# Performance work log

Hardware: AMD Instinct MI355X
Metric: run time of the kernel (lower is better)

The kernel has to match this reference:

```python
import math
import jax, jax.numpy as jnp
import numpy as np

NUM_HEADS = 16
NUM_LANDMARKS = 64
INV_ITERS = 6
ATT_SIZE = 1024
HEAD_SIZE = ATT_SIZE // NUM_HEADS  # dk = 64
NEG = -100000.0


def moore_penrose_pinv(x, num_iter):
    # lucidrains-style iterative Moore-Penrose pseudo-inverse
    abs_x = jnp.abs(x)
    col = abs_x.sum(axis=-1)
    row = abs_x.sum(axis=-2)
    z = jnp.swapaxes(x, -1, -2) / (jnp.max(col) * jnp.max(row))
    I = jnp.eye(x.shape[-1], dtype=x.dtype)
    for _ in range(num_iter):
        xz = x @ z
        z = 0.25 * z @ (13.0 * I - xz @ (15.0 * I - xz @ (7.0 * I - xz)))
    return z


def masked_softmax_scores(k, q, mask):
    # q @ k^T (dk=1: q already scaled) + mask, softmax over last dim
    s = jnp.einsum('bhmd,bhld->bhml', q, k)
    if mask is not None:
        s = s + (1.0 - mask) * NEG
    return jax.nn.softmax(s, axis=-1)


def setup_inputs() -> dict:
    key = jax.random.key(0)
    k1, k2, k3 = jax.random.split(key, 3)
    B, L, D = 4, 4096, 1024
    x = jax.random.normal(k1, (B, L, D), dtype=jnp.float32)
    attention_mask = jnp.ones((B, L), dtype=jnp.float32)
    w_kqv = jax.random.normal(k2, (3 * ATT_SIZE, D), dtype=jnp.float32) * 0.02
    w_out = jax.random.normal(k3, (ATT_SIZE, ATT_SIZE), dtype=jnp.float32) * 0.02
    b_out = jnp.zeros((ATT_SIZE,), dtype=jnp.float32)
    return {"x": x, "attention_mask": attention_mask,
            "w_kqv": w_kqv, "w_out": w_out, "b_out": b_out}


def reference(x, attention_mask, w_kqv, w_out, b_out):
    B, L, D = x.shape
    H, nl, hd = NUM_HEADS, NUM_LANDMARKS, HEAD_SIZE
    seg = L // nl  # landmark segment length (L already a multiple of nl)

    kqv = x @ w_kqv.T  # [B, L, 3A]
    k, q, v = jnp.split(kqv, 3, axis=-1)
    split = lambda t: t.reshape(B, L, H, hd).transpose(0, 2, 1, 3)  # [B,H,L,hd]
    k, q, v = split(k), split(q), split(v)

    mask = attention_mask[:, None, :]  # [B,1,L]
    denom = mask.reshape(B, 1, nl, seg).sum(-1) + 1e-08  # [B,1,nl]
    mask_lm = (denom > 0).astype(x.dtype)  # [B,1,nl]
    denom4 = denom[..., None]              # [B,1,nl,1]
    maskL = mask[..., None]                # [B,1,L,1]

    q = q * maskL
    k = k * maskL
    v = v * maskL

    s1_mask = maskL * mask_lm[..., None, :]               # [B,1,L,nl]
    s2_mask = mask_lm[..., None] * mask_lm[..., None, :]  # [B,1,nl,nl]
    s3_mask = jnp.swapaxes(s1_mask, -1, -2)               # [B,1,nl,L]

    q = q / math.sqrt(HEAD_SIZE)
    q_lm = q.reshape(B, H, nl, seg, hd).sum(-2) / denom4  # [B,H,nl,hd]
    k_lm = k.reshape(B, H, nl, seg, hd).sum(-2) / denom4

    scores_1 = masked_softmax_scores(k_lm, q, s1_mask)     # [B,H,L,nl]
    scores_2 = masked_softmax_scores(k_lm, q_lm, s2_mask)  # [B,H,nl,nl]
    scores_3 = masked_softmax_scores(k, q_lm, s3_mask)     # [B,H,nl,L]

    z_star = moore_penrose_pinv(scores_2, INV_ITERS)       # [B,H,nl,nl]
    out = scores_1 @ (z_star @ (scores_3 @ v))             # [B,H,L,hd]

    out = out.transpose(0, 2, 1, 3).reshape(B, L, H * hd)  # merge heads
    return out @ w_out.T + b_out
```

## Files before the change

kernel.cpp:

```cpp
#include <hip/hip_runtime.h>
#include <hip/hip_bf16.h>


static constexpr int Bn  = 4;
static constexpr int Ln  = 4096;
static constexpr int Dn  = 1024;
static constexpr int Hn  = 16;
static constexpr int HDn = 64;
static constexpr int NLn = 64;
static constexpr int SEGn = 64;
static constexpr int BHn = Bn * Hn;
static constexpr int Mn  = Bn * Ln;
static constexpr int NCH = 8;
#define NEG_BIG (-100000.0f)

static constexpr size_t OFF_KT  = 0;
static constexpr size_t OFF_QT  = 16777216;
static constexpr size_t OFF_VT  = 33554432;
static constexpr size_t OFF_WOH = 33554432;
static constexpr size_t OFF_WH  = 50331648;
static constexpr size_t OFF_QLM = 50331648;
static constexpr size_t OFF_KLM = 50593792;
static constexpr size_t OFF_S2  = 50855936;
static constexpr size_t OFF_Z   = 51118080;
static constexpr size_t OFF_WM  = 51380224;
static constexpr size_t OFF_PM  = 51642368;
static constexpr size_t OFF_PS  = 51675136;
static constexpr size_t OFF_GM  = 51707904;
static constexpr size_t OFF_XS  = 53477376;
static constexpr size_t OFF_PO  = 53477376;

using bf16x8 = __attribute__((ext_vector_type(8))) short;
using f32x16 = __attribute__((ext_vector_type(16))) float;
using s16x4  = __attribute__((ext_vector_type(4))) short;

__device__ __forceinline__ unsigned short f2bf(float f) {
    unsigned int u = __float_as_uint(f);
    return (unsigned short)((u + 0x7fffu + ((u >> 16) & 1u)) >> 16);
}
__device__ __forceinline__ void cvt8r(const float* fs, bf16x8& hv) {
    #pragma unroll
    for (int e = 0; e < 8; ++e) hv[e] = (short)f2bf(fs[e]);
}
typedef __attribute__((address_space(1))) void gvoid;
typedef __attribute__((address_space(3))) void lvoid;
__device__ __forceinline__ void async16(void* l, const void* g) {
    __builtin_amdgcn_global_load_lds((gvoid*)(size_t)g, (lvoid*)l, 16, 0, 0);
}

__global__ __launch_bounds__(256) void k_pack(
    const float* __restrict__ src, unsigned short* __restrict__ dh, int row0)
{
    __shared__ float Ls[128][33];
    const int rt = blockIdx.x, kt = blockIdx.y;
    const int tid = threadIdx.x;
    #pragma unroll
    for (int p = 0; p < 4; ++p) {
        const int row = p * 32 + (tid >> 3);
        const int c4 = (tid & 7) * 4;
        const float4 v = *(const float4*)&src[(size_t)(row0 + rt * 128 + row) * 1024 + kt * 32 + c4];
        Ls[row][c4 + 0] = v.x; Ls[row][c4 + 1] = v.y;
        Ls[row][c4 + 2] = v.z; Ls[row][c4 + 3] = v.w;
    }
    __syncthreads();
    const size_t tb = (size_t)(rt * 32 + kt) * 4096;
    for (int s = tid; s < 512; s += 256) {
        const int g = s >> 7, kk = (s >> 6) & 1, l = s & 63;
        const int row = g * 32 + (l & 31);
        const int k0 = kk * 16 + ((l >> 5) & 1) * 8;
        bf16x8 hv;
        cvt8r(&Ls[row][k0], hv);
        *(bf16x8*)&dh[tb + s * 8] = hv;
    }
}

#define GEMM4W_CORE(A_, B_, NNB)                                               \
    __shared__ __attribute__((aligned(16))) char smem[16384];                  \
    const int tid = threadIdx.x;                                               \
    const int lane = tid & 63, wid = tid >> 6;                                 \
    const int cpx = gridDim.x >> 3;                                            \
    const int wg = (blockIdx.x & 7) * cpx + (blockIdx.x >> 3);                 \
    const int bm = wg / (NNB), bn = wg % (NNB);                                \
    const int wrow = wid >> 1, wcol = wid & 1;                                 \
    const unsigned short* gsrc =                                               \
        (wid < 2 ? (A_) + (size_t)bm * 131072 : (B_) + (size_t)bn * 131072)    \
        + (wid & 1) * 2048 + lane * 8;                                         \
    char* ldst = smem + wid * 4096;                                            \
    f32x16 acc[2][2] = {};                                                     \
    for (int kt = 0; kt < 32; ++kt) {                                          \
        const unsigned short* g = gsrc + (size_t)kt * 4096;                    \
        __syncthreads();                                                       \
        _Pragma("unroll")                                                      \
        for (int i = 0; i < 4; ++i)                                            \
            async16(ldst + i * 1024, g + i * 512);                             \
        __syncthreads();                                                       \
        _Pragma("unroll")                                                      \
        for (int kk = 0; kk < 2; ++kk) {                                       \
            bf16x8 fa[2], fb[2];                                               \
            _Pragma("unroll")                                                  \
            for (int ti = 0; ti < 2; ++ti) {                                   \
                const int o = (((wrow * 2 + ti) * 2 + kk) << 10) + lane * 16;  \
                fa[ti] = *(const bf16x8*)(smem + o);                           \
            }                                                                  \
            _Pragma("unroll")                                                  \
            for (int tj = 0; tj < 2; ++tj) {                                   \
                const int o = (((wcol * 2 + tj) * 2 + kk) << 10) + lane * 16;  \
                fb[tj] = *(const bf16x8*)(smem + 8192 + o);                    \
            }                                                                  \
            _Pragma("unroll")                                                  \
            for (int ti = 0; ti < 2; ++ti)                                     \
                _Pragma("unroll")                                              \
                for (int tj = 0; tj < 2; ++tj)                                 \
                    acc[ti][tj] = __builtin_amdgcn_mfma_f32_32x32x16_bf16(     \
                        fa[ti], fb[tj], acc[ti][tj], 0, 0, 0);                 \
        }                                                                      \
    }

__global__ __launch_bounds__(256) void k_kqv_gemm(
    const unsigned short* __restrict__ xh,
    const unsigned short* __restrict__ wh,
    const float* __restrict__ mask,
    float* __restrict__ Kt, float* __restrict__ Qt, float* __restrict__ Vt,
    int row0)
{
    GEMM4W_CORE(xh, wh, 24)
    const int part = bn >> 3;
    #pragma unroll
    for (int ti = 0; ti < 2; ++ti) {
        #pragma unroll
        for (int tj = 0; tj < 2; ++tj) {
            const int col = (bn * 128 + wcol * 64 + tj * 32 + (lane & 31)) & 1023;
            const int h = col >> 6, d = col & 63;
            #pragma unroll
            for (int r = 0; r < 16; ++r) {
                const int row = row0 + bm * 128 + wrow * 64 + ti * 32
                              + (r & 3) + 8 * (r >> 2) + 4 * (lane >> 5);
                const int b = row >> 12, l = row & 4095;
                const float mk = mask[b * Ln + l];
                const size_t idx = ((size_t)(b * Hn + h) * Ln + l) * HDn + d;
                const float v = acc[ti][tj][r] * mk;
                if (part == 0)      Kt[idx] = v;
                else if (part == 1) Qt[idx] = v * 0.125f;
                else                Vt[idx] = v;
            }
        }
    }
}

__global__ __launch_bounds__(256) void k_out_gemm(
    const unsigned short* __restrict__ ah_,
    const unsigned short* __restrict__ bh_,
    const float* __restrict__ bias, float* __restrict__ out)
{
    GEMM4W_CORE(ah_, bh_, 8)
    #pragma unroll
    for (int ti = 0; ti < 2; ++ti) {
        #pragma unroll
        for (int tj = 0; tj < 2; ++tj) {
            const int col = bn * 128 + wcol * 64 + tj * 32 + (lane & 31);
            const float bb = bias[col];
            #pragma unroll
            for (int r = 0; r < 16; ++r) {
                const int row = bm * 128 + wrow * 64 + ti * 32
                              + (r & 3) + 8 * (r >> 2) + 4 * (lane >> 5);
                out[(size_t)row * Dn + col] = acc[ti][tj][r] + bb;
            }
        }
    }
}

__global__ __launch_bounds__(64) void k_landmarks(
    const float* __restrict__ Kt, const float* __restrict__ Qt,
    const float* __restrict__ mask,
    float* __restrict__ klm, float* __restrict__ qlm, int* __restrict__ gmax)
{
    const int blk = blockIdx.x;
    const int m = blk & 63, bh = blk >> 6, b = bh >> 4;
    const int d = threadIdx.x;
    if (blk == 0 && d < 2) gmax[d] = 0;
    float mv = mask[b * Ln + m * SEGn + d];
    #pragma unroll
    for (int off = 32; off; off >>= 1) mv += __shfl_down(mv, off);
    const float denom = __shfl(mv, 0) + 1e-8f;
    const float* kp = Kt + ((size_t)bh * Ln + m * SEGn) * HDn + d;
    const float* qp = Qt + ((size_t)bh * Ln + m * SEGn) * HDn + d;
    float sk = 0.f, sq = 0.f;
    for (int j = 0; j < SEGn; ++j) {
        sk += kp[(size_t)j * HDn];
        sq += qp[(size_t)j * HDn];
    }
    klm[((size_t)bh * NLn + m) * HDn + d] = sk / denom;
    qlm[((size_t)bh * NLn + m) * HDn + d] = sq / denom;
}

__global__ __launch_bounds__(64) void k_s2(
    const float* __restrict__ qlm, const float* __restrict__ klm,
    float* __restrict__ s2, int* __restrict__ gmax)
{
    const int bh = blockIdx.x;
    __shared__ float ql[64][65];
    __shared__ float kl[64][65];
    __shared__ float sr[64][65];
    const int t = threadIdx.x;
    for (int idx = t; idx < 4096; idx += 64) {
        ql[idx >> 6][idx & 63] = qlm[(size_t)bh * 4096 + idx];
        kl[idx >> 6][idx & 63] = klm[(size_t)bh * 4096 + idx];
    }
    __syncthreads();
    float mx = -1e30f;
    for (int mp = 0; mp < 64; ++mp) {
        float s = 0.f;
        #pragma unroll 8
        for (int d2 = 0; d2 < 64; ++d2) s = fmaf(ql[t][d2], kl[mp][d2], s);
        sr[t][mp] = s;
        mx = fmaxf(mx, s);
    }
    float sum = 0.f;
    for (int mp = 0; mp < 64; ++mp) {
        const float e = expf(sr[t][mp] - mx);
        sr[t][mp] = e;
        sum += e;
    }
    const float inv = 1.f / sum;
    float rs = 0.f;
    for (int mp = 0; mp < 64; ++mp) {
        const float v = sr[t][mp] * inv;
        sr[t][mp] = v;
        s2[(size_t)bh * 4096 + t * 64 + mp] = v;
        rs += fabsf(v);
    }
    __syncthreads();
    float cs = 0.f;
    for (int mm = 0; mm < 64; ++mm) cs += fabsf(sr[mm][t]);
    float rmax = rs, cmax = cs;
    #pragma unroll
    for (int off = 32; off; off >>= 1) {
        rmax = fmaxf(rmax, __shfl_down(rmax, off));
        cmax = fmaxf(cmax, __shfl_down(cmax, off));
    }
    if (t == 0) {
        atomicMax(&gmax[0], __float_as_int(rmax));
        atomicMax(&gmax[1], __float_as_int(cmax));
    }
}

template<int SUB>
__device__ __forceinline__ void mm64v(
    float* C, int ldc, const float* Ag, int lda,
    const float* Bm, int ldb, float dg, float scl)
{
    const int tid = threadIdx.x;
    const int tx = tid & 15, ty = tid >> 4;
    const int i0 = ty << 2, j0 = tx << 2;
    float acc[4][4] = {};
    for (int k0 = 0; k0 < 64; k0 += 4) {
        float4 a4[4], b4[4];
        #pragma unroll
        for (int i = 0; i < 4; ++i)
            a4[i] = *(const float4*)&Ag[(size_t)(i0 + i) * lda + k0];
        #pragma unroll
        for (int kk = 0; kk < 4; ++kk)
            b4[kk] = *(const float4*)&Bm[(size_t)(k0 + kk) * ldb + j0];
        if (SUB) {
            #pragma unroll
            for (int kk = 0; kk < 4; ++kk) {
                float* bp = (float*)&b4[kk];
                #pragma unroll
                for (int j = 0; j < 4; ++j)
                    bp[j] = ((k0 + kk == j0 + j) ? dg : 0.0f) - bp[j];
            }
        }
        #pragma unroll
        for (int i = 0; i < 4; ++i) {
            const float* ap = (const float*)&a4[i];
            #pragma unroll
            for (int kk = 0; kk < 4; ++kk) {
                const float* bp = (const float*)&b4[kk];
                #pragma unroll
                for (int j = 0; j < 4; ++j)
                    acc[i][j] = fmaf(ap[kk], bp[j], acc[i][j]);
            }
        }
    }
    __syncthreads();
    #pragma unroll
    for (int i = 0; i < 4; ++i)
        #pragma unroll
        for (int j = 0; j < 4; ++j) C[(size_t)(i0 + i) * ldc + j0 + j] = scl * acc[i][j];
    __syncthreads();
}

__global__ __launch_bounds__(256) void k_pinv_s3v(
    const float* __restrict__ s2, const int* __restrict__ gmax,
    float* __restrict__ zout,
    const float* __restrict__ qlm, const float* __restrict__ Kt,
    const float* __restrict__ Vt, const float* __restrict__ mask,
    float* __restrict__ Opart, float* __restrict__ mpart, float* __restrict__ spart)
{
    __shared__ __attribute__((aligned(16))) char shm[61184];
    const int tid = threadIdx.x;

    if (blockIdx.y == NCH) {
        float (*Zb)[68] = (float(*)[68])(shm);
        float (*XZ)[68] = (float(*)[68])(shm + 17408);
        float (*Tb)[68] = (float(*)[68])(shm + 34816);
        const int bh = blockIdx.x;
        const float* X = s2 + (size_t)bh * 4096;
        const float scale = 1.0f / (__int_as_float(gmax[0]) * __int_as_float(gmax[1]));
        for (int idx = tid; idx < 4096; idx += 256) {
            const int i = idx >> 6, j = idx & 63;
            Zb[i][j] = X[j * 64 + i] * scale;
        }
        __syncthreads();
        for (int it = 0; it < 6; ++it) {
            mm64v<0>(&XZ[0][0], 68, X, 64, &Zb[0][0], 68, 0.f, 1.f);
            mm64v<1>(&Tb[0][0], 68, &XZ[0][0], 68, &XZ[0][0], 68, 7.f, 1.f);
            mm64v<1>(&Tb[0][0], 68, &XZ[0][0], 68, &Tb[0][0], 68, 15.f, 1.f);
            mm64v<1>(&Zb[0][0], 68, &Zb[0][0], 68, &Tb[0][0], 68, 13.f, 0.25f);
        }
        for (int idx = tid; idx < 4096; idx += 256)
            zout[(size_t)bh * 4096 + idx] = Zb[idx >> 6][idx & 63];
        return;
    }

    float (*Sm)[65] = (float(*)[65])(shm);
    float (*Ks)[65] = (float(*)[65])(shm + 16640);
    float (*Vs)[65] = (float(*)[65])(shm + 33280);
    unsigned short* Qp = (unsigned short*)(shm + 49920);
    float (*red)[4]  = (float(*)[4])(shm + 58112);
    float (*red2)[4] = (float(*)[4])(shm + 59136);
    float* rowmax = (float*)(shm + 60160);
    float* rowsum = (float*)(shm + 60416);
    float* fac    = (float*)(shm + 60672);
    float* mrow   = (float*)(shm + 60928);
    const int bh = blockIdx.x, ch = blockIdx.y;
    const int b = bh >> 4;
    const int lane = tid & 63, wid = tid >> 6;
    const int wr = wid >> 1, wc = wid & 1;

    for (int idx = tid; idx < 4096; idx += 256)
        Sm[idx >> 6][idx & 63] = qlm[(size_t)bh * 4096 + idx];
    if (tid < 64) { rowmax[tid] = -1e30f; rowsum[tid] = 0.f; }
    __syncthreads();
    for (int s = tid; s < 512; s += 256) {
        const int g = s >> 8, kc = (s >> 6) & 3, l = s & 63;
        const int row = g * 32 + (l & 31);
        const int k0 = kc * 16 + ((l >> 5) & 1) * 8;
        bf16x8 hv;
        cvt8r(&Sm[row][k0], hv);
        *(bf16x8*)&Qp[s * 8] = hv;
    }
    f32x16 accO = {};
    const int t0beg = ch * (Ln / NCH), t0end = t0beg + (Ln / NCH);
    for (int t0 = t0beg; t0 < t0end; t0 += 64) {
        __syncthreads();
        for (int idx = tid; idx < 4096; idx += 256) {
            const int r = idx >> 6, c2 = idx & 63;
            Ks[r][c2] = Kt[((size_t)bh * Ln + t0 + r) * HDn + c2];
            Vs[r][c2] = Vt[((size_t)bh * Ln + t0 + r) * HDn + c2];
        }
        if (tid < 64) mrow[tid] = mask[b * Ln + t0 + tid];
        __syncthreads();
        f32x16 acc = {};
        #pragma unroll
        for (int kc = 0; kc < 4; ++kc) {
            const bf16x8 a_h = *(const bf16x8*)&Qp[((wr * 4 + kc) * 64 + lane) * 8];
            const int brow = wc * 32 + (lane & 31);
            const int k0 = kc * 16 + (lane >> 5) * 8;
            bf16x8 b_h;
            cvt8r(&Ks[brow][k0], b_h);
            acc = __builtin_amdgcn_mfma_f32_32x32x16_bf16(a_h, b_h, acc, 0, 0, 0);
        }
        #pragma unroll
        for (int r = 0; r < 16; ++r) {
            const int row = wr * 32 + (r & 3) + 8 * (r >> 2) + 4 * (lane >> 5);
            const int col = wc * 32 + (lane & 31);
            Sm[row][col] = acc[r] + (1.f - mrow[col]) * NEG_BIG;
        }
        __syncthreads();
        {
            const int row = tid >> 2, sg = tid & 3, c0 = sg * 16;
            float mx = -1e30f;
            #pragma unroll
            for (int c = 0; c < 16; ++c) mx = fmaxf(mx, Sm[row][c0 + c]);
            red[row][sg] = mx;
            __syncthreads();
            const float nm = fmaxf(rowmax[row],
                fmaxf(fmaxf(red[row][0], red[row][1]), fmaxf(red[row][2], red[row][3])));
            const float f = __expf(rowmax[row] - nm);
            float ps = 0.f;
            #pragma unroll
            for (int c = 0; c < 16; ++c) {
                const float e = __expf(Sm[row][c0 + c] - nm);
                Sm[row][c0 + c] = e;
                ps += e;
            }
            red2[row][sg] = ps;
            __syncthreads();
            if (sg == 0) {
                rowsum[row] = rowsum[row] * f
                    + red2[row][0] + red2[row][1] + red2[row][2] + red2[row][3];
                rowmax[row] = nm;
                fac[row] = f;
            }
        }
        __syncthreads();
        #pragma unroll
        for (int r = 0; r < 16; ++r) {
            const int row = wr * 32 + (r & 3) + 8 * (r >> 2) + 4 * (lane >> 5);
            accO[r] *= fac[row];
        }
        #pragma unroll
        for (int kc = 0; kc < 4; ++kc) {
            const int arow = wr * 32 + (lane & 31);
            const int ak0 = kc * 16 + (lane >> 5) * 8;
            bf16x8 a_h;
            cvt8r(&Sm[arow][ak0], a_h);
            const int bcol = wc * 32 + (lane & 31);
            const int bk0 = kc * 16 + (lane >> 5) * 8;
            float bw[8];
            #pragma unroll
            for (int e = 0; e < 8; ++e) bw[e] = Vs[bk0 + e][bcol];
            bf16x8 b_h;
            cvt8r(bw, b_h);
            accO = __builtin_amdgcn_mfma_f32_32x32x16_bf16(a_h, b_h, accO, 0, 0, 0);
        }
    }
    __syncthreads();
    #pragma unroll
    for (int r = 0; r < 16; ++r) {
        const int row = wr * 32 + (r & 3) + 8 * (r >> 2) + 4 * (lane >> 5);
        Vs[row][wc * 32 + (lane & 31)] = accO[r];
    }
    __syncthreads();
    const size_t ob = (size_t)(bh * NCH + ch) * 4096;
    for (int idx = tid; idx < 4096; idx += 256)
        Opart[ob + idx] = Vs[idx >> 6][idx & 63];
    if (tid < 64) {
        mpart[(bh * NCH + ch) * 64 + tid] = rowmax[tid];
        spart[(bh * NCH + ch) * 64 + tid] = rowsum[tid];
    }
}

__global__ __launch_bounds__(256) void k_mergez(
    const float* __restrict__ Opart, const float* __restrict__ mpart,
    const float* __restrict__ spart, const float* __restrict__ Zs,
    float* __restrict__ Wm)
{
    __shared__ float Sv[64][68];
    __shared__ float Zb[64][68];
    const int bh = blockIdx.x, tid = threadIdx.x;
    for (int idx = tid; idx < 4096; idx += 256)
        Zb[idx >> 6][idx & 63] = Zs[(size_t)bh * 4096 + idx];
    {
        const int r = tid >> 2, c0 = (tid & 3) * 16;
        float e[NCH];
        float M = -1e30f;
        #pragma unroll
        for (int c = 0; c < NCH; ++c) {
            e[c] = mpart[(bh * NCH + c) * 64 + r];
            M = fmaxf(M, e[c]);
        }
        float S = 0.f;
        #pragma unroll
        for (int c = 0; c < NCH; ++c) {
            e[c] = expf(e[c] - M);
            S += spart[(bh * NCH + c) * 64 + r] * e[c];
        }
        const float invS = 1.f / S;
        for (int col = c0; col < c0 + 16; ++col) {
            float o = 0.f;
            #pragma unroll
            for (int c = 0; c < NCH; ++c)
                o += Opart[(size_t)(bh * NCH + c) * 4096 + r * 64 + col] * e[c];
            Sv[r][col] = o * invS;
        }
    }
    __syncthreads();
    const int tx = tid & 15, ty = tid >> 4;
    const int i0 = ty << 2, j0 = tx << 2;
    float acc[4][4] = {};
    for (int k0 = 0; k0 < 64; k0 += 4) {
        float4 a4[4], b4[4];
        #pragma unroll
        for (int i = 0; i < 4; ++i)
            a4[i] = *(const float4*)&Zb[i0 + i][k0];
        #pragma unroll
        for (int kk = 0; kk < 4; ++kk)
            b4[kk] = *(const float4*)&Sv[k0 + kk][j0];
        #pragma unroll
        for (int i = 0; i < 4; ++i) {
            const float* ap = (const float*)&a4[i];
            #pragma unroll
            for (int kk = 0; kk < 4; ++kk) {
                const float* bp = (const float*)&b4[kk];
                #pragma unroll
                for (int j = 0; j < 4; ++j)
                    acc[i][j] = fmaf(ap[kk], bp[j], acc[i][j]);
            }
        }
    }
    #pragma unroll
    for (int i = 0; i < 4; ++i)
        #pragma unroll
        for (int j = 0; j < 4; ++j)
            Wm[(size_t)bh * 4096 + (i0 + i) * 64 + j0 + j] = acc[i][j];
}

__global__ __launch_bounds__(256) void k_attn_out(
    const float* __restrict__ Qt, const float* __restrict__ klm,
    const float* __restrict__ Wm, unsigned short* __restrict__ ah)
{
    const int lt = blockIdx.x;
    const int bh = blockIdx.y;
    const int b = bh >> 4, h = bh & 15;
    __shared__ float Sm[64][65];
    __shared__ float Ks[64][65];
    __shared__ float Ws[64][65];
    __shared__ unsigned short Qp[4096];
    __shared__ float red[64][4], red2[64][4];
    __shared__ float invr[64];
    const int tid = threadIdx.x;
    const int lane = tid & 63, wid = tid >> 6;
    const int wr = wid >> 1, wc = wid & 1;

    for (int idx = tid; idx < 4096; idx += 256) {
        const int r = idx >> 6, c2 = idx & 63;
        Sm[r][c2] = Qt[((size_t)bh * Ln + lt * 64 + r) * HDn + c2];
        Ks[r][c2] = klm[(size_t)bh * 4096 + idx];
        Ws[r][c2] = Wm[(size_t)bh * 4096 + idx];
    }
    __syncthreads();
    for (int s = tid; s < 512; s += 256) {
        const int g = s >> 8, kc = (s >> 6) & 3, l = s & 63;
        const int row = g * 32 + (l & 31);
        const int k0 = kc * 16 + ((l >> 5) & 1) * 8;
        bf16x8 hv;
        cvt8r(&Sm[row][k0], hv);
        *(bf16x8*)&Qp[s * 8] = hv;
    }
    __syncthreads();
    f32x16 acc = {};
    #pragma unroll
    for (int kc = 0; kc < 4; ++kc) {
        const bf16x8 a_h = *(const bf16x8*)&Qp[((wr * 4 + kc) * 64 + lane) * 8];
        const int brow = wc * 32 + (lane & 31);
        const int k0 = kc * 16 + (lane >> 5) * 8;
        bf16x8 b_h;
        cvt8r(&Ks[brow][k0], b_h);
        acc = __builtin_amdgcn_mfma_f32_32x32x16_bf16(a_h, b_h, acc, 0, 0, 0);
    }
    #pragma unroll
    for (int r = 0; r < 16; ++r) {
        const int row = wr * 32 + (r & 3) + 8 * (r >> 2) + 4 * (lane >> 5);
        Sm[row][wc * 32 + (lane & 31)] = acc[r];
    }
    __syncthreads();
    {
        const int row = tid >> 2, sg = tid & 3, c0 = sg * 16;
        float mx = -1e30f;
        #pragma unroll
        for (int c = 0; c < 16; ++c) mx = fmaxf(mx, Sm[row][c0 + c]);
        red[row][sg] = mx;
        __syncthreads();
        mx = fmaxf(fmaxf(red[row][0], red[row][1]), fmaxf(red[row][2], red[row][3]));
        float ps = 0.f;
        #pragma unroll
        for (int c = 0; c < 16; ++c) {
            const float e = __expf(Sm[row][c0 + c] - mx);
            Sm[row][c0 + c] = e;
            ps += e;
        }
        red2[row][sg] = ps;
        __syncthreads();
        if (sg == 0)
            invr[row] = 1.f / (red2[row][0] + red2[row][1] + red2[row][2] + red2[row][3]);
    }
    __syncthreads();
    f32x16 acc2 = {};
    #pragma unroll
    for (int kc = 0; kc < 4; ++kc) {
        const int arow = wr * 32 + (lane & 31);
        const int ak0 = kc * 16 + (lane >> 5) * 8;
        bf16x8 a_h;
        cvt8r(&Sm[arow][ak0], a_h);
        const int bcol = wc * 32 + (lane & 31);
        const int bk0 = kc * 16 + (lane >> 5) * 8;
        float bw[8];
        #pragma unroll
        for (int e = 0; e < 8; ++e) bw[e] = Ws[bk0 + e][bcol];
        bf16x8 b_h;
        cvt8r(bw, b_h);
        acc2 = __builtin_amdgcn_mfma_f32_32x32x16_bf16(a_h, b_h, acc2, 0, 0, 0);
    }
    __syncthreads();
    #pragma unroll
    for (int r = 0; r < 16; ++r) {
        const int row = wr * 32 + (r & 3) + 8 * (r >> 2) + 4 * (lane >> 5);
        Ks[row][wc * 32 + (lane & 31)] = acc2[r];
    }
    __syncthreads();
    const int tx = tid & 15, ty = tid >> 4;
    const int i0 = ty << 2, j0 = tx << 2;
    const int kd = h * 64 + j0;
    const int kt2 = kd >> 5, kc2 = kd & 31;
    const int kk2 = kc2 >> 4, half = (kc2 & 15) >> 3, e0 = kc2 & 7;
    #pragma unroll
    for (int i = 0; i < 4; ++i) {
        const float inv = invr[i0 + i];
        const int gm = b * Ln + lt * 64 + i0 + i;
        const int mt = gm >> 7, g2 = (gm & 127) >> 5, lrow = gm & 31;
        const size_t u = (size_t)(mt * 32 + kt2) * 4096
                       + (size_t)(((g2 * 2 + kk2) * 64 + half * 32 + lrow) * 8 + e0);
        s16x4 hv;
        #pragma unroll
        for (int j = 0; j < 4; ++j)
            hv[j] = (short)f2bf(Ks[i0 + i][j0 + j] * inv);
        *(s16x4*)&ah[u] = hv;
    }
}

extern "C" void kernel_launch(void* const* d_in, const int* in_sizes, int n_in,
                              void* d_out, int out_size, void* d_ws, size_t ws_size,
                              hipStream_t stream)
{
    (void)in_sizes; (void)n_in; (void)out_size;
    const float* x    = (const float*)d_in[0];
    const float* mask = (const float*)d_in[1];
    const float* wkqv = (const float*)d_in[2];
    const float* wout = (const float*)d_in[3];
    const float* bout = (const float*)d_in[4];
    float* out = (float*)d_out;
    float* ws  = (float*)d_ws;

    float* Kt   = ws + OFF_KT;
    float* Qt   = ws + OFF_QT;
    float* Vt   = ws + OFF_VT;
    float* qlm  = ws + OFF_QLM;
    float* klm  = ws + OFF_KLM;
    float* s2   = ws + OFF_S2;
    float* zst  = ws + OFF_Z;
    float* Wm   = ws + OFF_WM;
    int*   gmax = (int*)(ws + OFF_GM);
    float* mpart = ws + OFF_PM;
    float* spart = ws + OFF_PS;
    float* Opart = ws + OFF_PO;
    unsigned short* wh  = (unsigned short*)(ws + OFF_WH);
    unsigned short* woh = (unsigned short*)(ws + OFF_WOH);
    unsigned short* attn_h = (unsigned short*)(ws + OFF_KT);

    int S = 2048;
    if (ws_size >= (size_t)(OFF_XS + 16384 * 512) * 4) S = 16384;
    else if (ws_size >= (size_t)(OFF_XS + 8192 * 512) * 4) S = 8192;
    else if (ws_size >= (size_t)(OFF_XS + 2097152) * 4) S = 4096;
    unsigned short* xhs = (unsigned short*)(ws + OFF_XS);

    k_pack<<<dim3(24, 32), 256, 0, stream>>>(wkqv, wh, 0);
    for (int s = 0; s < Mn / S; ++s) {
        k_pack<<<dim3(S / 128, 32), 256, 0, stream>>>(x, xhs, s * S);
        k_kqv_gemm<<<(S / 128) * 24, 256, 0, stream>>>(
            xhs, wh, mask, Kt, Qt, Vt, s * S);
    }
    k_landmarks<<<BHn * NLn, 64, 0, stream>>>(Kt, Qt, mask, klm, qlm, gmax);
    k_s2<<<BHn, 64, 0, stream>>>(qlm, klm, s2, gmax);
    k_pinv_s3v<<<dim3(BHn, NCH + 1), 256, 0, stream>>>(
        s2, gmax, zst, qlm, Kt, Vt, mask, Opart, mpart, spart);
    k_pack<<<dim3(8, 32), 256, 0, stream>>>(wout, woh, 0);
    k_mergez<<<BHn, 256, 0, stream>>>(Opart, mpart, spart, zst, Wm);
    k_attn_out<<<dim3(Ln / 64, BHn), 256, 0, stream>>>(Qt, klm, Wm, attn_h);
    k_out_gemm<<<128 * 8, 256, 0, stream>>>(attn_h, woh, bout, out);
}
```

Before: 435.5 us.

## Parallelize s2 softmax over 256 threads and amortize attn_out tile loads

k_s2 now runs 256 threads per head, with four threads sharing each row and partial max, sum and abs-sum values reduced through shared memory. It also switches to the fast __expf. k_attn_out processes four 64-row L tiles per block, so the landmark-key and W tiles are loaded into shared memory once per four tiles instead of once per tile. This cuts redundant global loads and launch count, but leaves four times fewer blocks (1024) and adds an extra shared buffer, which may lower occupancy.

```diff
diff --git a/kernel.cpp b/kernel.cpp
--- a/kernel.cpp
+++ b/kernel.cpp
@@ -193,7 +193,7 @@
     qlm[((size_t)bh * NLn + m) * HDn + d] = sq / denom;
 }
 
-__global__ __launch_bounds__(64) void k_s2(
+__global__ __launch_bounds__(256) void k_s2(
     const float* __restrict__ qlm, const float* __restrict__ klm,
     float* __restrict__ s2, int* __restrict__ gmax)
 {
@@ -201,46 +201,69 @@
     __shared__ float ql[64][65];
     __shared__ float kl[64][65];
     __shared__ float sr[64][65];
-    const int t = threadIdx.x;
-    for (int idx = t; idx < 4096; idx += 64) {
+    __shared__ float red[64][4], red2[64][4];
+    __shared__ float rtmp[64], ctmp[64];
+    const int tid = threadIdx.x;
+    for (int idx = tid; idx < 4096; idx += 256) {
         ql[idx >> 6][idx & 63] = qlm[(size_t)bh * 4096 + idx];
         kl[idx >> 6][idx & 63] = klm[(size_t)bh * 4096 + idx];
     }
     __syncthreads();
+    const int row = tid >> 2, sg = tid & 3, c0 = sg * 16;
+    float sv[16];
     float mx = -1e30f;
-    for (int mp = 0; mp < 64; ++mp) {
+    #pragma unroll 4
+    for (int m = 0; m < 16; ++m) {
         float s = 0.f;
         #pragma unroll 8
-        for (int d2 = 0; d2 < 64; ++d2) s = fmaf(ql[t][d2], kl[mp][d2], s);
-        sr[t][mp] = s;
+        for (int d2 = 0; d2 < 64; ++d2) s = fmaf(ql[row][d2], kl[c0 + m][d2], s);
+        sv[m] = s;
         mx = fmaxf(mx, s);
     }
+    red[row][sg] = mx;
+    __syncthreads();
+    mx = fmaxf(fmaxf(red[row][0], red[row][1]), fmaxf(red[row][2], red[row][3]));
     float sum = 0.f;
-    for (int mp = 0; mp < 64; ++mp) {
-        const float e = expf(sr[t][mp] - mx);
-        sr[t][mp] = e;
+    #pragma unroll
+    for (int m = 0; m < 16; ++m) {
+        const float e = __expf(sv[m] - mx);
+        sv[m] = e;
         sum += e;
     }
-    const float inv = 1.f / sum;
+    red2[row][sg] = sum;
+    __syncthreads();
+    const float inv = 1.f / (red2[row][0] + red2[row][1] + red2[row][2] + red2[row][3]);
     float rs = 0.f;
-    for (int mp = 0; mp < 64; ++mp) {
-        const float v = sr[t][mp] * inv;
-        sr[t][mp] = v;
-        s2[(size_t)bh * 4096 + t * 64 + mp] = v;
+    #pragma unroll
+    for (int m = 0; m < 16; ++m) {
+        const float v = sv[m] * inv;
+        sr[row][c0 + m] = v;
+        s2[(size_t)bh * 4096 + row * 64 + c0 + m] = v;
         rs += fabsf(v);
     }
-    __syncthreads();
+    red[row][sg] = rs;
+    __syncthreads();
+    if (sg == 0)
+        rtmp[row] = red[row][0] + red[row][1] + red[row][2] + red[row][3];
     float cs = 0.f;
-    for (int mm = 0; mm < 64; ++mm) cs += fabsf(sr[mm][t]);
-    float rmax = rs, cmax = cs;
-    #pragma unroll
-    for (int off = 32; off; off >>= 1) {
-        rmax = fmaxf(rmax, __shfl_down(rmax, off));
-        cmax = fmaxf(cmax, __shfl_down(cmax, off));
-    }
-    if (t == 0) {
-        atomicMax(&gmax[0], __float_as_int(rmax));
-        atomicMax(&gmax[1], __float_as_int(cmax));
+    #pragma unroll
+    for (int r = 0; r < 16; ++r) cs += fabsf(sr[c0 + r][row]);
+    red2[row][sg] = cs;
+    __syncthreads();
+    if (sg == 0)
+        ctmp[row] = red2[row][0] + red2[row][1] + red2[row][2] + red2[row][3];
+    __syncthreads();
+    if (tid < 64) {
+        float rmax = rtmp[tid], cmax = ctmp[tid];
+        #pragma unroll
+        for (int off = 32; off; off >>= 1) {
+            rmax = fmaxf(rmax, __shfl_down(rmax, off));
+            cmax = fmaxf(cmax, __shfl_down(cmax, off));
+        }
+        if (tid == 0) {
+            atomicMax(&gmax[0], __float_as_int(rmax));
+            atomicMax(&gmax[1], __float_as_int(cmax));
+        }
     }
 }
 
@@ -511,12 +534,13 @@
     const float* __restrict__ Qt, const float* __restrict__ klm,
     const float* __restrict__ Wm, unsigned short* __restrict__ ah)
 {
-    const int lt = blockIdx.x;
+    const int lt0 = blockIdx.x * 4;
     const int bh = blockIdx.y;
     const int b = bh >> 4, h = bh & 15;
     __shared__ float Sm[64][65];
     __shared__ float Ks[64][65];
     __shared__ float Ws[64][65];
+    __shared__ float Ob[64][65];
     __shared__ unsigned short Qp[4096];
     __shared__ float red[64][4], red2[64][4];
     __shared__ float invr[64];
@@ -526,97 +550,106 @@
 
     for (int idx = tid; idx < 4096; idx += 256) {
         const int r = idx >> 6, c2 = idx & 63;
-        Sm[r][c2] = Qt[((size_t)bh * Ln + lt * 64 + r) * HDn + c2];
         Ks[r][c2] = klm[(size_t)bh * 4096 + idx];
         Ws[r][c2] = Wm[(size_t)bh * 4096 + idx];
     }
     __syncthreads();
-    for (int s = tid; s < 512; s += 256) {
-        const int g = s >> 8, kc = (s >> 6) & 3, l = s & 63;
-        const int row = g * 32 + (l & 31);
-        const int k0 = kc * 16 + ((l >> 5) & 1) * 8;
-        bf16x8 hv;
-        cvt8r(&Sm[row][k0], hv);
-        *(bf16x8*)&Qp[s * 8] = hv;
-    }
-    __syncthreads();
-    f32x16 acc = {};
-    #pragma unroll
-    for (int kc = 0; kc < 4; ++kc) {
-        const bf16x8 a_h = *(const bf16x8*)&Qp[((wr * 4 + kc) * 64 + lane) * 8];
-        const int brow = wc * 32 + (lane & 31);
-        const int k0 = kc * 16 + (lane >> 5) * 8;
-        bf16x8 b_h;
-        cvt8r(&Ks[brow][k0], b_h);
-        acc = __builtin_amdgcn_mfma_f32_32x32x16_bf16(a_h, b_h, acc, 0, 0, 0);
-    }
-    #pragma unroll
-    for (int r = 0; r < 16; ++r) {
-        const int row = wr * 32 + (r & 3) + 8 * (r >> 2) + 4 * (lane >> 5);
-        Sm[row][wc * 32 + (lane & 31)] = acc[r];
-    }
-    __syncthreads();
-    {
-        const int row = tid >> 2, sg = tid & 3, c0 = sg * 16;
-        float mx = -1e30f;
-        #pragma unroll
-        for (int c = 0; c < 16; ++c) mx = fmaxf(mx, Sm[row][c0 + c]);
-        red[row][sg] = mx;
-        __syncthreads();
-        mx = fmaxf(fmaxf(red[row][0], red[row][1]), fmaxf(red[row][2], red[row][3]));
-        float ps = 0.f;
-        #pragma unroll
-        for (int c = 0; c < 16; ++c) {
-            const float e = __expf(Sm[row][c0 + c] - mx);
-            Sm[row][c0 + c] = e;
-            ps += e;
-        }
-        red2[row][sg] = ps;
-        __syncthreads();
-        if (sg == 0)
-            invr[row] = 1.f / (red2[row][0] + red2[row][1] + red2[row][2] + red2[row][3]);
-    }
-    __syncthreads();
-    f32x16 acc2 = {};
-    #pragma unroll
-    for (int kc = 0; kc < 4; ++kc) {
-        const int arow = wr * 32 + (lane & 31);
-        const int ak0 = kc * 16 + (lane >> 5) * 8;
-        bf16x8 a_h;
-        cvt8r(&Sm[arow][ak0], a_h);
-        const int bcol = wc * 32 + (lane & 31);
-        const int bk0 = kc * 16 + (lane >> 5) * 8;
-        float bw[8];
-        #pragma unroll
-        for (int e = 0; e < 8; ++e) bw[e] = Ws[bk0 + e][bcol];
-        bf16x8 b_h;
-        cvt8r(bw, b_h);
-        acc2 = __builtin_amdgcn_mfma_f32_32x32x16_bf16(a_h, b_h, acc2, 0, 0, 0);
-    }
-    __syncthreads();
-    #pragma unroll
-    for (int r = 0; r < 16; ++r) {
-        const int row = wr * 32 + (r & 3) + 8 * (r >> 2) + 4 * (lane >> 5);
-        Ks[row][wc * 32 + (lane & 31)] = acc2[r];
-    }
-    __syncthreads();
-    const int tx = tid & 15, ty = tid >> 4;
-    const int i0 = ty << 2, j0 = tx << 2;
-    const int kd = h * 64 + j0;
-    const int kt2 = kd >> 5, kc2 = kd & 31;
-    const int kk2 = kc2 >> 4, half = (kc2 & 15) >> 3, e0 = kc2 & 7;
-    #pragma unroll
-    for (int i = 0; i < 4; ++i) {
-        const float inv = invr[i0 + i];
-        const int gm = b * Ln + lt * 64 + i0 + i;
-        const int mt = gm >> 7, g2 = (gm & 127) >> 5, lrow = gm & 31;
-        const size_t u = (size_t)(mt * 32 + kt2) * 4096
-                       + (size_t)(((g2 * 2 + kk2) * 64 + half * 32 + lrow) * 8 + e0);
-        s16x4 hv;
-        #pragma unroll
-        for (int j = 0; j < 4; ++j)
-            hv[j] = (short)f2bf(Ks[i0 + i][j0 + j] * inv);
-        *(s16x4*)&ah[u] = hv;
+
+    for (int sub = 0; sub < 4; ++sub) {
+        const int lt = lt0 + sub;
+        for (int idx = tid; idx < 4096; idx += 256)
+            Sm[idx >> 6][idx & 63] = Qt[((size_t)bh * Ln + lt * 64 + (idx >> 6)) * HDn + (idx & 63)];
+        __syncthreads();
+        for (int s = tid; s < 512; s += 256) {
+            const int g = s >> 8, kc = (s >> 6) & 3, l = s & 63;
+            const int row = g * 32 + (l & 31);
+            const int k0 = kc * 16 + ((l >> 5) & 1) * 8;
+            bf16x8 hv;
+            cvt8r(&Sm[row][k0], hv);
+            *(bf16x8*)&Qp[s * 8] = hv;
+        }
+        __syncthreads();
+        f32x16 acc = {};
+        #pragma unroll
+        for (int kc = 0; kc < 4; ++kc) {
+            const bf16x8 a_h = *(const bf16x8*)&Qp[((wr * 4 + kc) * 64 + lane) * 8];
+            const int brow = wc * 32 + (lane & 31);
+            const int k0 = kc * 16 + (lane >> 5) * 8;
+            bf16x8 b_h;
+            cvt8r(&Ks[brow][k0], b_h);
+            acc = __builtin_amdgcn_mfma_f32_32x32x16_bf16(a_h, b_h, acc, 0, 0, 0);
+        }
+        #pragma unroll
+        for (int r = 0; r < 16; ++r) {
+            const int row = wr * 32 + (r & 3) + 8 * (r >> 2) + 4 * (lane >> 5);
+            Sm[row][wc * 32 + (lane & 31)] = acc[r];
+        }
+        __syncthreads();
+        {
+            const int row = tid >> 2, sg = tid & 3, c0 = sg * 16;
+            float mx = -1e30f;
+            #pragma unroll
+            for (int c = 0; c < 16; ++c) mx = fmaxf(mx, Sm[row][c0 + c]);
+            red[row][sg] = mx;
+            __syncthreads();
+            mx = fmaxf(fmaxf(red[row][0], red[row][1]), fmaxf(red[row][2], red[row][3]));
+            float ps = 0.f;
+            #pragma unroll
+            for (int c = 0; c < 16; ++c) {
+                const float e = __expf(Sm[row][c0 + c] - mx);
+                Sm[row][c0 + c] = e;
+                ps += e;
+            }
+            red2[row][sg] = ps;
+            __syncthreads();
+            if (sg == 0)
+                invr[row] = 1.f / (red2[row][0] + red2[row][1] + red2[row][2] + red2[row][3]);
+        }
+        __syncthreads();
+        f32x16 acc2 = {};
+        #pragma unroll
+        for (int kc = 0; kc < 4; ++kc) {
+            const int arow = wr * 32 + (lane & 31);
+            const int ak0 = kc * 16 + (lane >> 5) * 8;
+            bf16x8 a_h;
+            cvt8r(&Sm[arow][ak0], a_h);
+            const int bcol = wc * 32 + (lane & 31);
+            const int bk0 = kc * 16 + (lane >> 5) * 8;
+            float bw[8];
+            #pragma unroll
+            for (int e = 0; e < 8; ++e) bw[e] = Ws[bk0 + e][bcol];
+            bf16x8 b_h;
+            cvt8r(bw, b_h);
+            acc2 = __builtin_amdgcn_mfma_f32_32x32x16_bf16(a_h, b_h, acc2, 0, 0, 0);
+        }
+        __syncthreads();
+        #pragma unroll
+        for (int r = 0; r < 16; ++r) {
+            const int row = wr * 32 + (r & 3) + 8 * (r >> 2) + 4 * (lane >> 5);
+            Ob[row][wc * 32 + (lane & 31)] = acc2[r];
+        }
+        __syncthreads();
+        {
+            const int tx = tid & 15, ty = tid >> 4;
+            const int i0 = ty << 2, j0 = tx << 2;
+            const int kd = h * 64 + j0;
+            const int kt2 = kd >> 5, kc2 = kd & 31;
+            const int kk2 = kc2 >> 4, half = (kc2 & 15) >> 3, e0 = kc2 & 7;
+            #pragma unroll
+            for (int i = 0; i < 4; ++i) {
+                const float inv = invr[i0 + i];
+                const int gm = b * Ln + lt * 64 + i0 + i;
+                const int mt = gm >> 7, g2 = (gm & 127) >> 5, lrow = gm & 31;
+                const size_t u = (size_t)(mt * 32 + kt2) * 4096
+                               + (size_t)(((g2 * 2 + kk2) * 64 + half * 32 + lrow) * 8 + e0);
+                s16x4 hv;
+                #pragma unroll
+                for (int j = 0; j < 4; ++j)
+                    hv[j] = (short)f2bf(Ob[i0 + i][j0 + j] * inv);
+                *(s16x4*)&ah[u] = hv;
+            }
+        }
+        __syncthreads();
     }
 }
 
@@ -662,11 +695,11 @@
             xhs, wh, mask, Kt, Qt, Vt, s * S);
     }
     k_landmarks<<<BHn * NLn, 64, 0, stream>>>(Kt, Qt, mask, klm, qlm, gmax);
-    k_s2<<<BHn, 64, 0, stream>>>(qlm, klm, s2, gmax);
+    k_s2<<<BHn, 256, 0, stream>>>(qlm, klm, s2, gmax);
     k_pinv_s3v<<<dim3(BHn, NCH + 1), 256, 0, stream>>>(
         s2, gmax, zst, qlm, Kt, Vt, mask, Opart, mpart, spart);
     k_pack<<<dim3(8, 32), 256, 0, stream>>>(wout, woh, 0);
     k_mergez<<<BHn, 256, 0, stream>>>(Opart, mpart, spart, zst, Wm);
-    k_attn_out<<<dim3(Ln / 64, BHn), 256, 0, stream>>>(Qt, klm, Wm, attn_h);
+    k_attn_out<<<dim3(Ln / 256, BHn), 256, 0, stream>>>(Qt, klm, Wm, attn_h);
     k_out_gemm<<<128 * 8, 256, 0, stream>>>(attn_h, woh, bout, out);
 }
```

New measurement: 402.5 us. 1.08x faster.
